# Kernel optimization log

Hardware: AMD Instinct MI355X
Metric: run time of the kernel (lower is better)

Reference implementation:

```python
import jax, jax.numpy as jnp
import numpy as np

M, N, D = 100000, 64, 128  # points, channels, voxel grid side


def setup_inputs() -> dict:
    key = jax.random.key(0)
    k1, k2, k3, k4, k5 = jax.random.split(key, 5)
    rng = np.random.default_rng(0)
    # unique occupied voxels in a D^3 grid (Minkowski coords are unique)
    lin = rng.choice(D ** 3, size=M, replace=False)
    coords = np.stack(np.unravel_index(lin, (D, D, D)), axis=1).astype(np.int32)
    w_scale = 0.02  # ~1/sqrt(fan_in=27*N)
    return {
        "feats": jax.random.normal(k1, (M, N), dtype=jnp.float32),
        "W1": jax.random.normal(k2, (27, N, N), dtype=jnp.float32) * w_scale,
        "b1": jax.random.normal(k3, (N,), dtype=jnp.float32) * 0.01,
        "W2": jax.random.normal(k4, (27, N, N), dtype=jnp.float32) * w_scale,
        "b2": jax.random.normal(k5, (N,), dtype=jnp.float32) * 0.01,
        "coords": jnp.asarray(coords),
        "grid_size": D,
    }


def reference(feats, W1, b1, W2, b2, coords, grid_size):
    Dg = grid_size
    m = feats.shape[0]
    # dense hash: linear voxel id -> point index (-1 if empty)
    lin = (coords[:, 0].astype(jnp.int32) * Dg + coords[:, 1]) * Dg + coords[:, 2]
    lookup = jnp.full((Dg * Dg * Dg,), -1, dtype=jnp.int32).at[lin].set(
        jnp.arange(m, dtype=jnp.int32))
    offsets = jnp.array([[i, j, k] for i in (-1, 0, 1) for j in (-1, 0, 1)
                         for k in (-1, 0, 1)], dtype=jnp.int32)  # [27,3]

    def sparse_conv(x, W, b):
        # out[u] = b + sum_k W_k^T gather(x, u+off_k); scan over 27 offsets keeps
        # only one [M,N] gathered buffer live (memory-bound gather-GEMM-scatter)
        def step(acc, wk_off):
            W_k, off = wk_off
            nc = coords + off  # [M,3]
            inb = jnp.all((nc >= 0) & (nc < Dg), axis=1)
            nlin = (nc[:, 0] * Dg + nc[:, 1]) * Dg + nc[:, 2]
            nidx = lookup[jnp.where(inb, nlin, 0)]
            valid = inb & (nidx >= 0)
            g = jnp.where(valid[:, None], x[jnp.maximum(nidx, 0)], 0.0)  # [M,N]
            return acc + g @ W_k, None
        init = jnp.zeros_like(x) + b
        out, _ = jax.lax.scan(step, init, (W, offsets))
        return out

    h = jax.nn.relu(sparse_conv(feats, W1, b1))
    return jax.nn.relu(sparse_conv(h, W2, b2))
```

## Files before the change

### kernel.cpp

```cpp
#include <hip/hip_runtime.h>
#include <hip/hip_bf16.h>
#include <cstdint>
#include <cstddef>

typedef _Float16 half8 __attribute__((ext_vector_type(8)));
typedef float floatx16 __attribute__((ext_vector_type(16)));

#define DGRID 128
#define D3 (DGRID * DGRID * DGRID)
#define WSZ (2 * 27 * 4096)

struct __attribute__((aligned(4))) I3 { int a, b, c; };

__global__ void prep(const int* __restrict__ coords, const float* __restrict__ feats,
                     const float* __restrict__ W1, const float* __restrict__ W2,
                     int* __restrict__ lookup, _Float16* __restrict__ Whf,
                     _Float16* __restrict__ h0, _Float16* __restrict__ h, int M) {
    int tid = blockIdx.x * 256 + threadIdx.x;
    if (tid < WSZ) {
        int idx = tid;
        int j = idx & 7;
        int l = (idx >> 3) & 63;
        int f = (idx >> 9) & 7;
        int kL = idx >> 12;
        int k = kL % 27, L = kL / 27;
        int kk = f & 3, ct = f >> 2;
        int c = kk * 16 + (l >> 5) * 8 + j;
        int n = ct * 32 + (l & 31);
        const float* W = L ? W2 : W1;
        Whf[idx] = (_Float16)W[k * 4096 + c * 64 + n];
        return;
    }
    tid -= WSZ;
    if (tid < M) {
        int x = coords[3 * tid], y = coords[3 * tid + 1], z = coords[3 * tid + 2];
        lookup[(x * DGRID + y) * DGRID + z] = tid;
        return;
    }
    tid -= M;
    if (tid < 64) {
        h0[(size_t)M * 64 + tid] = (_Float16)0.f;
        h[(size_t)M * 64 + tid] = (_Float16)0.f;
        return;
    }
    tid -= 64;
    if (tid < M * 8) {
        const float4* src = (const float4*)feats + (size_t)tid * 2;
        float4 f0 = src[0], f1 = src[1];
        half8 v;
        v[0] = (_Float16)f0.x; v[1] = (_Float16)f0.y;
        v[2] = (_Float16)f0.z; v[3] = (_Float16)f0.w;
        v[4] = (_Float16)f1.x; v[5] = (_Float16)f1.y;
        v[6] = (_Float16)f1.z; v[7] = (_Float16)f1.w;
        ((half8*)h0)[tid] = v;
    }
}

template <bool FIRST, bool OUT_F16>
__global__ __launch_bounds__(64, 2) void spconv(const _Float16* __restrict__ x,
                                                const _Float16* __restrict__ Whf,
                                                const float* __restrict__ bias,
                                                const int* __restrict__ coords,
                                                const int* __restrict__ lookup,
                                                int* __restrict__ nbr,
                                                void* __restrict__ outp, int M) {
    __shared__ int nvs[27 * 64];
    const int lane = threadIdx.x;
    const int lrow = lane & 31;
    const int lhalf = lane >> 5;
    const int mw = blockIdx.x * 64;

    {
        const int row = mw + lane;
        if constexpr (FIRST) {
            if (row < M) {
                int X = coords[3 * row], Y = coords[3 * row + 1], Z = coords[3 * row + 2];
                int zlo = Z - 1;
                if (zlo < 0) zlo = 0;
                if (zlo > DGRID - 3) zlo = DGRID - 3;
                const int zi = Z - zlo;
#pragma unroll
                for (int dx = -1; dx <= 1; ++dx)
#pragma unroll
                    for (int dy = -1; dy <= 1; ++dy) {
                        int nx = X + dx, ny = Y + dy;
                        int v0 = -1, v1 = -1, v2 = -1;
                        if (((unsigned)nx < DGRID) && ((unsigned)ny < DGRID)) {
                            I3 t = *(const I3*)(lookup + ((nx * DGRID + ny) * DGRID + zlo));
                            v0 = t.a; v1 = t.b; v2 = t.c;
                        }
#pragma unroll
                        for (int dz = -1; dz <= 1; ++dz) {
                            int zc = Z + dz;
                            int i = zi + dz;
                            int val = (i == 0) ? v0 : (i == 1) ? v1 : v2;
                            int nidx = M;
                            if (((unsigned)zc < DGRID) && ((unsigned)val < (unsigned)M))
                                nidx = val;
                            int k = (dx + 1) * 9 + (dy + 1) * 3 + (dz + 1);
                            nvs[k * 64 + lane] = nidx;
                            nbr[(size_t)k * M + row] = nidx;
                        }
                    }
            } else {
#pragma unroll
                for (int k = 0; k < 27; ++k) nvs[k * 64 + lane] = M;
            }
        } else {
            const int rc = row < M ? row : M - 1;
#pragma unroll
            for (int k = 0; k < 27; ++k) nvs[k * 64 + lane] = nbr[(size_t)k * M + rc];
        }
    }
    __syncthreads();

    floatx16 acc[4];
#pragma unroll
    for (int i = 0; i < 4; ++i)
#pragma unroll
        for (int j = 0; j < 16; ++j) acc[i][j] = 0.0f;

    const half8* wb = (const half8*)Whf + lane;

    auto loadB = [&](half8* dst, int k) {
#pragma unroll
        for (int f = 0; f < 8; ++f) dst[f] = wb[(k * 8 + f) * 64];
    };
    auto loadA = [&](half8* dst, int n0, int n1) {
        const half8* p0 = (const half8*)(x + (size_t)n0 * 64 + lhalf * 8);
        const half8* p1 = (const half8*)(x + (size_t)n1 * 64 + lhalf * 8);
#pragma unroll
        for (int kk = 0; kk < 4; ++kk) {
            dst[kk] = p0[kk * 2];
            dst[4 + kk] = p1[kk * 2];
        }
    };

    int nv0[4], nv1[4];
#pragma unroll
    for (int j = 0; j < 3; ++j) {
        nv0[j] = nvs[j * 64 + lrow];
        nv1[j] = nvs[j * 64 + 32 + lrow];
    }

    half8 Ar[3][8], Br[2][8];
    loadB(Br[0], 0);
    loadA(Ar[0], nv0[0], nv1[0]);
    loadA(Ar[1], nv0[1], nv1[1]);

#pragma unroll
    for (int i = 0; i < 27; ++i) {
        {
            int jn = i + 3;
            if (jn < 27) {
                nv0[jn & 3] = nvs[jn * 64 + lrow];
                nv1[jn & 3] = nvs[jn * 64 + 32 + lrow];
            }
        }
        if (i + 1 < 27) loadB(Br[(i + 1) & 1], i + 1);
        {
            int ja = i + 2;
            if (ja < 27) loadA(Ar[ja % 3], nv0[ja & 3], nv1[ja & 3]);
        }
        __builtin_amdgcn_sched_barrier(0);
        half8* A = Ar[i % 3];
        half8* B = Br[i & 1];
#pragma unroll
        for (int kk = 0; kk < 4; ++kk)
#pragma unroll
            for (int rt = 0; rt < 2; ++rt)
#pragma unroll
                for (int ct = 0; ct < 2; ++ct)
                    acc[rt * 2 + ct] = __builtin_amdgcn_mfma_f32_32x32x16_f16(
                        A[rt * 4 + kk], B[ct * 4 + kk], acc[rt * 2 + ct], 0, 0, 0);
    }

    const float bv0 = bias[lrow], bv1 = bias[32 + lrow];
#pragma unroll
    for (int rt = 0; rt < 2; ++rt)
#pragma unroll
        for (int ct = 0; ct < 2; ++ct) {
            const float bb = ct ? bv1 : bv0;
#pragma unroll
            for (int reg = 0; reg < 16; ++reg) {
                int row = (reg & 3) + 8 * (reg >> 2) + 4 * lhalf;
                int g = mw + rt * 32 + row;
                if (g < M) {
                    float v = acc[rt * 2 + ct][reg] + bb;
                    v = v > 0.f ? v : 0.f;
                    size_t off = (size_t)g * 64 + ct * 32 + lrow;
                    if constexpr (OUT_F16)
                        ((_Float16*)outp)[off] = (_Float16)v;
                    else
                        ((float*)outp)[off] = v;
                }
            }
        }
}

extern "C" void kernel_launch(void* const* d_in, const int* in_sizes, int n_in,
                              void* d_out, int out_size, void* d_ws, size_t ws_size,
                              hipStream_t stream) {
    const float* feats = (const float*)d_in[0];
    const float* W1 = (const float*)d_in[1];
    const float* b1 = (const float*)d_in[2];
    const float* W2 = (const float*)d_in[3];
    const float* b2 = (const float*)d_in[4];
    const int* coords = (const int*)d_in[5];
    const int M = in_sizes[0] / 64;

    int* lookup = (int*)d_ws;
    int* nbr = lookup + (size_t)D3;
    _Float16* h = (_Float16*)(nbr + (size_t)27 * M);
    _Float16* h0 = h + (size_t)(M + 1) * 64;
    _Float16* Whf = h0 + (size_t)(M + 1) * 64;
    size_t need = (size_t)D3 * 4 + (size_t)27 * M * 4 +
                  2 * (size_t)(M + 1) * 64 * 2 + (size_t)WSZ * 2;
    if (ws_size < need) return;

    long long pt = (long long)WSZ + M + 64 + (long long)M * 8;
    prep<<<(int)((pt + 255) / 256), 256, 0, stream>>>(coords, feats, W1, W2, lookup, Whf,
                                                      h0, h, M);

    int cb = (M + 63) / 64;
    spconv<true, true><<<cb, 64, 0, stream>>>(h0, Whf, b1, coords, lookup, nbr,
                                              (void*)h, M);
    spconv<false, false><<<cb, 64, 0, stream>>>(h, Whf + (size_t)27 * 4096, b2, coords,
                                                lookup, nbr, d_out, M);
}
```

Baseline: 171.7 us.

## Share weight tiles across four waves via LDS with async global-to-LDS loads

Blocks grow from one wave to four (256 threads), each wave still handling 64 rows. Per-offset weight tiles now go through a double-buffered LDS area filled by global_load_lds, so four waves share one copy instead of each wave loading its own B fragments from global memory. This cuts weight traffic per row and register pressure. In exchange it adds a block-wide barrier on every one of the 27 offsets, which can stall waves waiting on their irregular gather loads, and it raises LDS use per block.

```diff
diff --git a/kernel.cpp b/kernel.cpp
--- a/kernel.cpp
+++ b/kernel.cpp
@@ -57,21 +57,36 @@
 }
 
 template <bool FIRST, bool OUT_F16>
-__global__ __launch_bounds__(64, 2) void spconv(const _Float16* __restrict__ x,
-                                                const _Float16* __restrict__ Whf,
-                                                const float* __restrict__ bias,
-                                                const int* __restrict__ coords,
-                                                const int* __restrict__ lookup,
-                                                int* __restrict__ nbr,
-                                                void* __restrict__ outp, int M) {
-    __shared__ int nvs[27 * 64];
-    const int lane = threadIdx.x;
+__global__ __launch_bounds__(256, 2) void spconv(const _Float16* __restrict__ x,
+                                                 const _Float16* __restrict__ Whf,
+                                                 const float* __restrict__ bias,
+                                                 const int* __restrict__ coords,
+                                                 const int* __restrict__ lookup,
+                                                 int* __restrict__ nbr,
+                                                 void* __restrict__ outp, int M) {
+    __shared__ int nvs[27 * 256];
+    __shared__ _Float16 bsh[2][4096];
+    const int tid = threadIdx.x;
+    const int lane = tid & 63;
+    const int wid = tid >> 6;
     const int lrow = lane & 31;
     const int lhalf = lane >> 5;
-    const int mw = blockIdx.x * 64;
+    const int mw = blockIdx.x * 256;
+    const int wb0 = wid * 64;
 
     {
-        const int row = mw + lane;
+        const _Float16* src = Whf + (size_t)0 * 4096 + wid * 512 + lane * 8;
+        __builtin_amdgcn_global_load_lds(
+            (const __attribute__((address_space(1))) void*)src,
+            (__attribute__((address_space(3))) void*)&bsh[0][wid * 512], 16, 0, 0);
+        const _Float16* src2 = src + 2048;
+        __builtin_amdgcn_global_load_lds(
+            (const __attribute__((address_space(1))) void*)src2,
+            (__attribute__((address_space(3))) void*)&bsh[0][2048 + wid * 512], 16, 0, 0);
+    }
+
+    {
+        const int row = mw + tid;
         if constexpr (FIRST) {
             if (row < M) {
                 int X = coords[3 * row], Y = coords[3 * row + 1], Z = coords[3 * row + 2];
@@ -98,18 +113,18 @@
                             if (((unsigned)zc < DGRID) && ((unsigned)val < (unsigned)M))
                                 nidx = val;
                             int k = (dx + 1) * 9 + (dy + 1) * 3 + (dz + 1);
-                            nvs[k * 64 + lane] = nidx;
+                            nvs[k * 256 + tid] = nidx;
                             nbr[(size_t)k * M + row] = nidx;
                         }
                     }
             } else {
 #pragma unroll
-                for (int k = 0; k < 27; ++k) nvs[k * 64 + lane] = M;
+                for (int k = 0; k < 27; ++k) nvs[k * 256 + tid] = M;
             }
         } else {
             const int rc = row < M ? row : M - 1;
 #pragma unroll
-            for (int k = 0; k < 27; ++k) nvs[k * 64 + lane] = nbr[(size_t)k * M + rc];
+            for (int k = 0; k < 27; ++k) nvs[k * 256 + tid] = nbr[(size_t)k * M + rc];
         }
     }
     __syncthreads();
@@ -120,11 +135,20 @@
 #pragma unroll
         for (int j = 0; j < 16; ++j) acc[i][j] = 0.0f;
 
-    const half8* wb = (const half8*)Whf + lane;
-
-    auto loadB = [&](half8* dst, int k) {
-#pragma unroll
-        for (int f = 0; f < 8; ++f) dst[f] = wb[(k * 8 + f) * 64];
+    auto stageB = [&](int buf, int k) {
+        const _Float16* src = Whf + (size_t)k * 4096 + wid * 512 + lane * 8;
+        __builtin_amdgcn_global_load_lds(
+            (const __attribute__((address_space(1))) void*)src,
+            (__attribute__((address_space(3))) void*)&bsh[buf][wid * 512], 16, 0, 0);
+        const _Float16* src2 = src + 2048;
+        __builtin_amdgcn_global_load_lds(
+            (const __attribute__((address_space(1))) void*)src2,
+            (__attribute__((address_space(3))) void*)&bsh[buf][2048 + wid * 512], 16, 0, 0);
+    };
+    auto readB = [&](half8* dst, int buf) {
+#pragma unroll
+        for (int f = 0; f < 8; ++f)
+            dst[f] = *(const half8*)&bsh[buf][f * 512 + lane * 8];
     };
     auto loadA = [&](half8* dst, int n0, int n1) {
         const half8* p0 = (const half8*)(x + (size_t)n0 * 64 + lhalf * 8);
@@ -139,32 +163,33 @@
     int nv0[4], nv1[4];
 #pragma unroll
     for (int j = 0; j < 3; ++j) {
-        nv0[j] = nvs[j * 64 + lrow];
-        nv1[j] = nvs[j * 64 + 32 + lrow];
-    }
-
-    half8 Ar[3][8], Br[2][8];
-    loadB(Br[0], 0);
+        nv0[j] = nvs[j * 256 + wb0 + lrow];
+        nv1[j] = nvs[j * 256 + wb0 + 32 + lrow];
+    }
+
+    half8 Ar[3][8];
     loadA(Ar[0], nv0[0], nv1[0]);
     loadA(Ar[1], nv0[1], nv1[1]);
 
 #pragma unroll
     for (int i = 0; i < 27; ++i) {
+        if (i + 1 < 27) stageB((i + 1) & 1, i + 1);
         {
             int jn = i + 3;
             if (jn < 27) {
-                nv0[jn & 3] = nvs[jn * 64 + lrow];
-                nv1[jn & 3] = nvs[jn * 64 + 32 + lrow];
+                nv0[jn & 3] = nvs[jn * 256 + wb0 + lrow];
+                nv1[jn & 3] = nvs[jn * 256 + wb0 + 32 + lrow];
             }
         }
-        if (i + 1 < 27) loadB(Br[(i + 1) & 1], i + 1);
         {
             int ja = i + 2;
             if (ja < 27) loadA(Ar[ja % 3], nv0[ja & 3], nv1[ja & 3]);
         }
+        half8 B[8];
+        readB(B, i & 1);
         __builtin_amdgcn_sched_barrier(0);
+        __syncthreads();
         half8* A = Ar[i % 3];
-        half8* B = Br[i & 1];
 #pragma unroll
         for (int kk = 0; kk < 4; ++kk)
 #pragma unroll
@@ -184,7 +209,7 @@
 #pragma unroll
             for (int reg = 0; reg < 16; ++reg) {
                 int row = (reg & 3) + 8 * (reg >> 2) + 4 * lhalf;
-                int g = mw + rt * 32 + row;
+                int g = mw + wb0 + rt * 32 + row;
                 if (g < M) {
                     float v = acc[rt * 2 + ct][reg] + bb;
                     v = v > 0.f ? v : 0.f;
@@ -222,9 +247,9 @@
     prep<<<(int)((pt + 255) / 256), 256, 0, stream>>>(coords, feats, W1, W2, lookup, Whf,
                                                       h0, h, M);
 
-    int cb = (M + 63) / 64;
-    spconv<true, true><<<cb, 64, 0, stream>>>(h0, Whf, b1, coords, lookup, nbr,
-                                              (void*)h, M);
-    spconv<false, false><<<cb, 64, 0, stream>>>(h, Whf + (size_t)27 * 4096, b2, coords,
-                                                lookup, nbr, d_out, M);
+    int cb = (M + 255) / 256;
+    spconv<true, true><<<cb, 256, 0, stream>>>(h0, Whf, b1, coords, lookup, nbr,
+                                               (void*)h, M);
+    spconv<false, false><<<cb, 256, 0, stream>>>(h, Whf + (size_t)27 * 4096, b2, coords,
+                                                 lookup, nbr, d_out, M);
 }
```

Measured after the change: 168.4 us. Within noise of the previous version (-1.9%).
